# Optimization experiments

Measured on AMD Instinct MI355X. Metric: run time of the kernel, lower is better.

Reference implementation:

```python
import jax, jax.numpy as jnp
import numpy as np

EPS = 1e-5
H = 8  # num_heads


def _layernorm(x, g, b):
    m = x.mean(axis=-1, keepdims=True)
    v = jnp.mean((x - m) ** 2, axis=-1, keepdims=True)
    return (x - m) / jnp.sqrt(v + EPS) * g + b


def setup_inputs() -> dict:
    key = jax.random.key(0)
    ks = jax.random.split(key, 8)
    B, T, N, D, L = 4, 4096, 512, 1024, 768
    x = jax.random.normal(ks[0], (B, T, D), dtype=jnp.float32)
    cond = jax.random.normal(ks[1], (B, N, L), dtype=jnp.float32)
    # LayerNorm params
    ln_g = jnp.ones((D,), jnp.float32)
    ln_b = jnp.zeros((D,), jnp.float32)
    tln_g = jnp.ones((L,), jnp.float32)
    tln_b = jnp.zeros((L,), jnp.float32)
    # Linear params, stored as (in, out)
    Wq = jax.random.normal(ks[2], (D, D), jnp.float32) * 0.02
    bq = jnp.zeros((D,), jnp.float32)
    Wk = jax.random.normal(ks[3], (L, D), jnp.float32) * 0.02
    bk = jnp.zeros((D,), jnp.float32)
    Wv = jax.random.normal(ks[4], (L, D), jnp.float32) * 0.02
    bv = jnp.zeros((D,), jnp.float32)
    return {"input_tensor": x, "condition_tensor": cond,
            "ln_g": ln_g, "ln_b": ln_b, "tln_g": tln_g, "tln_b": tln_b,
            "Wq": Wq, "bq": bq, "Wk": Wk, "bk": bk, "Wv": Wv, "bv": bv}


def reference(input_tensor, condition_tensor, ln_g, ln_b, tln_g, tln_b,
              Wq, bq, Wk, bk, Wv, bv):
    B, T, D = input_tensor.shape
    N = condition_tensor.shape[1]
    xn = _layernorm(input_tensor, ln_g, ln_b)            # [B,T,D]
    cn = _layernorm(condition_tensor, tln_g, tln_b)      # [B,N,L]
    q = jnp.einsum('btd,de->bte', xn, Wq) + bq           # [B,T,D]
    k = jnp.einsum('bnl,ld->bnd', cn, Wk) + bk           # [B,N,D]
    v = jnp.einsum('bnl,ld->bnd', cn, Wv) + bv           # [B,N,D]
    q = jax.nn.softmax(q.reshape(B, T, H, D // H), axis=-1)  # softmax over head_dim
    k = jax.nn.softmax(k.reshape(B, N, H, D // H), axis=1)   # softmax over N
    v = v.reshape(B, N, H, D // H)
    context = jnp.einsum('bnhk,bnhv->bhkv', k, v)        # [B,H,hd,hd]
    y = jnp.einsum('bthk,bhkv->bthv', q, context).reshape(B, T, D)
    return y
```

## Files before the change

### kernel.cpp

```cpp
#include <hip/hip_runtime.h>
#include <hip/hip_bf16.h>
#include <stdint.h>

#define BATCH 4
#define TLEN  4096
#define DDIM  1024
#define NCOND 512
#define LDIM  768
#define NHEAD 8
#define HD    128

typedef __bf16 bf16x8 __attribute__((ext_vector_type(8)));
typedef float  f32x4  __attribute__((ext_vector_type(4)));

__device__ __forceinline__ unsigned short f2b(float f) {
    unsigned int u = __builtin_bit_cast(unsigned int, f);
    unsigned int r = (u + 0x7fffu + ((u >> 16) & 1u)) >> 16;
    return (unsigned short)r;
}
__device__ __forceinline__ float b2f(unsigned short s) {
    unsigned int u = ((unsigned int)s) << 16;
    return __builtin_bit_cast(float, u);
}

__device__ __forceinline__ void gl2lds(const void* g, void* l) {
    __builtin_amdgcn_global_load_lds(
        (const __attribute__((address_space(1))) void*)(uintptr_t)g,
        (__attribute__((address_space(3))) void*)(uintptr_t)l,
        16, 0, 0);
}

template<int NCH>
__device__ __forceinline__ void ln_row(const float* __restrict__ x,
    const float* __restrict__ g, const float* __restrict__ bb,
    unsigned short* __restrict__ o, long r, int lane)
{
    const int rowlen = NCH * 256;
    const float* p = x + r * (long)rowlen;
    float4 v[NCH];
    float s = 0.f, ss = 0.f;
#pragma unroll
    for (int i = 0; i < NCH; i++) {
        v[i] = *(const float4*)(p + i * 256 + lane * 4);
        s  += v[i].x + v[i].y + v[i].z + v[i].w;
        ss += v[i].x * v[i].x + v[i].y * v[i].y + v[i].z * v[i].z + v[i].w * v[i].w;
    }
#pragma unroll
    for (int off = 32; off; off >>= 1) {
        s  += __shfl_xor(s,  off, 64);
        ss += __shfl_xor(ss, off, 64);
    }
    float mu = s / rowlen;
    float rs = rsqrtf(fmaxf(ss / rowlen - mu * mu, 0.f) + 1e-5f);
    unsigned short* po = o + r * (long)rowlen;
#pragma unroll
    for (int i = 0; i < NCH; i++) {
        int c = i * 256 + lane * 4;
        float4 gv = *(const float4*)(g + c);
        float4 bv = *(const float4*)(bb + c);
        ushort4 o4;
        o4.x = f2b((v[i].x - mu) * rs * gv.x + bv.x);
        o4.y = f2b((v[i].y - mu) * rs * gv.y + bv.y);
        o4.z = f2b((v[i].z - mu) * rs * gv.z + bv.z);
        o4.w = f2b((v[i].w - mu) * rs * gv.w + bv.w);
        *(ushort4*)(po + c) = o4;
    }
}

__global__ __launch_bounds__(256) void prep(
    const float* __restrict__ x, const float* __restrict__ ln_g,
    const float* __restrict__ ln_b,
    const float* __restrict__ cond, const float* __restrict__ tln_g,
    const float* __restrict__ tln_b,
    const float* __restrict__ Wq, const float* __restrict__ Wk,
    const float* __restrict__ Wv,
    unsigned short* __restrict__ xn, unsigned short* __restrict__ cn,
    unsigned short* __restrict__ wqT, unsigned short* __restrict__ wkvT)
{
    int blk = blockIdx.x;
    int tid = threadIdx.x, wid = tid >> 6, lane = tid & 63;
    if (blk < 4096) {
        ln_row<4>(x, ln_g, ln_b, xn, (long)blk * 4 + wid, lane);
        return;
    }
    if (blk < 4608) {
        ln_row<3>(cond, tln_g, tln_b, cn, (long)(blk - 4096) * 4 + wid, lane);
        return;
    }
    int w = blk - 4608;
    const float* W; unsigned short* Wt; int K, wi;
    if (w < 1024)      { W = Wq; Wt = wqT;               K = DDIM; wi = w; }
    else if (w < 1792) { W = Wk; Wt = wkvT;              K = LDIM; wi = w - 1024; }
    else               { W = Wv; Wt = wkvT + 768 * 1024; K = LDIM; wi = w - 1792; }
    int n0 = (wi & 31) * 32, k0 = (wi >> 5) * 32;
    __shared__ float t[32][33];
    int tx = tid & 31, ty = tid >> 5;
#pragma unroll
    for (int i = 0; i < 4; i++)
        t[ty + i * 8][tx] = W[(long)(k0 + ty + i * 8) * DDIM + n0 + tx];
    __syncthreads();
#pragma unroll
    for (int i = 0; i < 4; i++)
        Wt[(long)(n0 + ty + i * 8) * K + k0 + tx] = f2b(t[tx][ty + i * 8]);
}

__global__ __launch_bounds__(256) void gemm_kv(
    const unsigned short* __restrict__ A,
    const unsigned short* __restrict__ Bt,
    const float* __restrict__ bk, const float* __restrict__ bv,
    float* __restrict__ Ck,
    unsigned short* __restrict__ Cvv)
{
    int zi = blockIdx.z;
    const unsigned short* Bp = Bt + (long)zi * 1024 * LDIM;
    const float* bias = zi ? bv : bk;

    int m0 = blockIdx.y * 128, n0 = blockIdx.x * 128;
    int tid = threadIdx.x, lane = tid & 63, wid = tid >> 6;
    int l16 = lane & 15, quad = lane >> 4;
    int mw = (wid & 1) << 6, nw = (wid >> 1) << 6;

    __shared__ unsigned short sb[16384];

    f32x4 acc[4][4];
#pragma unroll
    for (int i = 0; i < 4; i++)
#pragma unroll
        for (int j = 0; j < 4; j++) { acc[i][j][0] = 0.f; acc[i][j][1] = 0.f; acc[i][j][2] = 0.f; acc[i][j][3] = 0.f; }

    int cg = (tid & 3) ^ ((tid >> 3) & 3);
    const unsigned short* ag = A  + (long)(m0 + (tid >> 2)) * LDIM + cg * 8;
    const unsigned short* bg = Bp + (long)(n0 + (tid >> 2)) * LDIM + cg * 8;
    const long a64 = 64L * LDIM;
    int wsl = wid * 512;
    int sw = (l16 >> 1) & 3;

    auto stage = [&](unsigned short* d, int ko) {
        gl2lds(ag + ko,        d + wsl);
        gl2lds(ag + a64 + ko,  d + wsl + 2048);
        gl2lds(bg + ko,        d + 4096 + wsl);
        gl2lds(bg + a64 + ko,  d + 4096 + wsl + 2048);
    };

    const int NT = LDIM >> 5;
    stage(sb, 0);
    stage(sb + 8192, 32);

    for (int t = 0; t < NT; ++t) {
        if (t + 1 < NT) asm volatile("s_waitcnt vmcnt(4)" ::: "memory");
        else            asm volatile("s_waitcnt vmcnt(0)" ::: "memory");
        __builtin_amdgcn_s_barrier();
        __builtin_amdgcn_sched_barrier(0);
        unsigned short* Ac = sb + (t & 1) * 8192;
        bf16x8 af[4], bfr[4];
#pragma unroll
        for (int i = 0; i < 4; i++)
            af[i] = *(const bf16x8*)&Ac[(mw + i * 16 + l16) * 32 + ((quad ^ sw) * 8)];
#pragma unroll
        for (int j = 0; j < 4; j++)
            bfr[j] = *(const bf16x8*)&Ac[4096 + (nw + j * 16 + l16) * 32 + ((quad ^ sw) * 8)];
#pragma unroll
        for (int i = 0; i < 4; i++)
#pragma unroll
            for (int j = 0; j < 4; j++)
                acc[i][j] = __builtin_amdgcn_mfma_f32_16x16x32_bf16(af[i], bfr[j], acc[i][j], 0, 0, 0);
        __builtin_amdgcn_s_barrier();
        __builtin_amdgcn_sched_barrier(0);
        if (t + 2 < NT) stage(Ac, (t + 2) << 5);
    }

#pragma unroll
    for (int j = 0; j < 4; j++) {
        int col = n0 + nw + j * 16 + l16;
        float bvv = bias[col];
#pragma unroll
        for (int i = 0; i < 4; i++) {
            int row0 = m0 + mw + i * 16 + (quad << 2);
#pragma unroll
            for (int r = 0; r < 4; r++) {
                float val = acc[i][j][r] + bvv;
                long idx = (long)(row0 + r) * DDIM + col;
                if (zi == 0) Ck[idx]  = val;
                else         Cvv[idx] = f2b(val);
            }
        }
    }
}

__global__ __launch_bounds__(256) void ctx_mfma2s(const float* __restrict__ kraw,
    const unsigned short* __restrict__ v,
    unsigned short* __restrict__ ctxT)
{
    __shared__ unsigned short vT[128 * 72];
    __shared__ unsigned short kT[32 * 72];
    __shared__ float shm[8][33], shs[8][33];
    __shared__ float Mc[32], Sc[32];
    int kk0 = blockIdx.x * 32;
    int bh  = blockIdx.y;
    int b = bh >> 3, h = bh & 7;
    int tid = threadIdx.x, lane = tid & 63, wid = tid >> 6;
    int l16 = lane & 15, quad = lane >> 4;

    const float* kbase = kraw + (long)b * NCOND * DDIM + h * HD + kk0;

    {
        int c = tid & 31, seg = tid >> 5;
        float m = -1e30f, s = 0.f;
#pragma unroll 4
        for (int i = 0; i < 64; i++) {
            float val = kbase[(long)(seg * 64 + i) * DDIM + c];
            float nm = fmaxf(m, val);
            s = s * __expf(m - nm) + __expf(val - nm);
            m = nm;
        }
        shm[seg][c] = m; shs[seg][c] = s;
        __syncthreads();
        if (seg == 0) {
            float M = shm[0][c], S = shs[0][c];
#pragma unroll
            for (int t = 1; t < 8; t++) {
                float m2 = shm[t][c], s2 = shs[t][c];
                float nm = fmaxf(M, m2);
                S = S * __expf(M - nm) + s2 * __expf(m2 - nm);
                M = nm;
            }
            Mc[c] = M; Sc[c] = 1.f / S;
        }
        __syncthreads();
    }

    f32x4 acc[2][2];
#pragma unroll
    for (int i = 0; i < 2; i++)
#pragma unroll
        for (int j = 0; j < 2; j++) { acc[i][j][0] = 0.f; acc[i][j][1] = 0.f; acc[i][j][2] = 0.f; acc[i][j][3] = 0.f; }

    for (int s = 0; s < 8; s++) {
        int n0 = s * 64;
        const float* kp = kbase + (long)n0 * DDIM;
        const unsigned short* vp = v + (long)b * NCOND * DDIM + (long)n0 * DDIM + h * HD;
#pragma unroll
        for (int p = 0; p < 8; p++) {
            int e = p * 256 + tid;
            int nn = e >> 5, kk = e & 31;
            float val = __expf(kp[(long)nn * DDIM + kk] - Mc[kk]) * Sc[kk];
            kT[kk * 72 + nn] = f2b(val);
        }
#pragma unroll
        for (int p = 0; p < 16; p++) {
            int e = p * 256 + tid;
            int nn = e >> 6, v2 = (e & 63) * 2;
            unsigned int w = *(const unsigned int*)&vp[(long)nn * DDIM + v2];
            vT[v2 * 72 + nn]       = (unsigned short)w;
            vT[(v2 + 1) * 72 + nn] = (unsigned short)(w >> 16);
        }
        __syncthreads();
#pragma unroll
        for (int ks = 0; ks < 2; ks++) {
            bf16x8 af[2], bfr[2];
#pragma unroll
            for (int i = 0; i < 2; i++)
                af[i] = *(const bf16x8*)&vT[(wid * 32 + i * 16 + l16) * 72 + ks * 32 + quad * 8];
#pragma unroll
            for (int j = 0; j < 2; j++)
                bfr[j] = *(const bf16x8*)&kT[(j * 16 + l16) * 72 + ks * 32 + quad * 8];
#pragma unroll
            for (int i = 0; i < 2; i++)
#pragma unroll
                for (int j = 0; j < 2; j++)
                    acc[i][j] = __builtin_amdgcn_mfma_f32_16x16x32_bf16(af[i], bfr[j], acc[i][j], 0, 0, 0);
        }
        __syncthreads();
    }

    unsigned short* cp = ctxT + ((long)bh << 14);
#pragma unroll
    for (int i = 0; i < 2; i++)
#pragma unroll
        for (int j = 0; j < 2; j++)
#pragma unroll
            for (int r = 0; r < 4; r++)
                cp[(wid * 32 + i * 16 + quad * 4 + r) * 128 + kk0 + j * 16 + l16] =
                    f2b(acc[i][j][r]);
}

__global__ __launch_bounds__(256, 4) void qfused(
    const unsigned short* __restrict__ xn,
    const unsigned short* __restrict__ wqT,
    const float* __restrict__ bq,
    const unsigned short* __restrict__ ctxT,
    float* __restrict__ out)
{
    __shared__ unsigned short buf[18432];
    unsigned short* Pb = buf;
    float* redM = (float*)(buf + 17408);
    float* redS = redM + 256;

    int d = blockIdx.x;
    int xcd = d & 7, slot = d >> 3;
    int mtile = xcd * 16 + (slot >> 3);
    int head = slot & 7;
    int m0 = mtile * 128;
    int b  = m0 >> 12;
    int tid = threadIdx.x, lane = tid & 63, wid = tid >> 6;
    int l16 = lane & 15, quad = lane >> 4;
    int mw = (wid & 1) << 6, nw = (wid >> 1) << 6;
    int ch = wid >> 1;

    const unsigned short* cg2 = ctxT + ((long)(b * NHEAD + head) << 14);

    f32x4 acc[4][4];
#pragma unroll
    for (int i = 0; i < 4; i++)
#pragma unroll
        for (int j = 0; j < 4; j++) { acc[i][j][0] = 0.f; acc[i][j][1] = 0.f; acc[i][j][2] = 0.f; acc[i][j][3] = 0.f; }

    int cgs = (tid & 3) ^ ((tid >> 3) & 3);
    const unsigned short* ag = xn  + (long)(m0 + (tid >> 2)) * DDIM + cgs * 8;
    const unsigned short* bg = wqT + (long)(head * 128 + (tid >> 2)) * DDIM + cgs * 8;
    const long a64 = 64L * DDIM;
    int wsl = wid * 512;
    int sw = (l16 >> 1) & 3;

    auto stage = [&](unsigned short* dst, int ko) {
        gl2lds(ag + ko,        dst + wsl);
        gl2lds(ag + a64 + ko,  dst + wsl + 2048);
        gl2lds(bg + ko,        dst + 4096 + wsl);
        gl2lds(bg + a64 + ko,  dst + 4096 + wsl + 2048);
    };

    const int NT = DDIM >> 5;
    stage(buf, 0);
    stage(buf + 8192, 32);

    for (int t = 0; t < NT; ++t) {
        if (t + 1 < NT) asm volatile("s_waitcnt vmcnt(4)" ::: "memory");
        else            asm volatile("s_waitcnt vmcnt(0)" ::: "memory");
        __builtin_amdgcn_s_barrier();
        __builtin_amdgcn_sched_barrier(0);
        unsigned short* Ac = buf + (t & 1) * 8192;
        bf16x8 af[4], bfr[4];
#pragma unroll
        for (int i = 0; i < 4; i++)
            af[i] = *(const bf16x8*)&Ac[(mw + i * 16 + l16) * 32 + ((quad ^ sw) * 8)];
#pragma unroll
        for (int j = 0; j < 4; j++)
            bfr[j] = *(const bf16x8*)&Ac[4096 + (nw + j * 16 + l16) * 32 + ((quad ^ sw) * 8)];
        __builtin_amdgcn_s_setprio(1);
#pragma unroll
        for (int i = 0; i < 4; i++)
#pragma unroll
            for (int j = 0; j < 4; j++)
                acc[i][j] = __builtin_amdgcn_mfma_f32_16x16x32_bf16(af[i], bfr[j], acc[i][j], 0, 0, 0);
        __builtin_amdgcn_s_setprio(0);
        __builtin_amdgcn_s_barrier();
        __builtin_amdgcn_sched_barrier(0);
        if (t + 2 < NT) stage(Ac, (t + 2) << 5);
    }

    float bvv[4];
#pragma unroll
    for (int j = 0; j < 4; j++) bvv[j] = bq[head * 128 + nw + j * 16 + l16];
#pragma unroll
    for (int i = 0; i < 4; i++)
#pragma unroll
        for (int j = 0; j < 4; j++)
#pragma unroll
            for (int r = 0; r < 4; r++) acc[i][j][r] += bvv[j];

    float mx[4][4];
#pragma unroll
    for (int i = 0; i < 4; i++)
#pragma unroll
        for (int r = 0; r < 4; r++) {
            float m = acc[i][0][r];
            m = fmaxf(m, acc[i][1][r]);
            m = fmaxf(m, acc[i][2][r]);
            m = fmaxf(m, acc[i][3][r]);
            mx[i][r] = m;
        }
#pragma unroll
    for (int off = 1; off < 16; off <<= 1)
#pragma unroll
        for (int i = 0; i < 4; i++)
#pragma unroll
            for (int r = 0; r < 4; r++)
                mx[i][r] = fmaxf(mx[i][r], __shfl_xor(mx[i][r], off, 64));
    if (l16 == 0) {
#pragma unroll
        for (int i = 0; i < 4; i++)
#pragma unroll
            for (int r = 0; r < 4; r++)
                redM[ch * 128 + mw + i * 16 + quad * 4 + r] = mx[i][r];
    }
    __syncthreads();

    float sm[4][4];
#pragma unroll
    for (int i = 0; i < 4; i++)
#pragma unroll
        for (int r = 0; r < 4; r++) {
            int row = mw + i * 16 + quad * 4 + r;
            float M = fmaxf(redM[row], redM[128 + row]);
            float s = 0.f;
#pragma unroll
            for (int j = 0; j < 4; j++) {
                unsigned short eb = f2b(__expf(acc[i][j][r] - M));
                Pb[row * 136 + nw + j * 16 + l16] = eb;
                s += b2f(eb);
            }
            sm[i][r] = s;
        }
#pragma unroll
    for (int off = 1; off < 16; off <<= 1)
#pragma unroll
        for (int i = 0; i < 4; i++)
#pragma unroll
            for (int r = 0; r < 4; r++)
                sm[i][r] += __shfl_xor(sm[i][r], off, 64);
    if (l16 == 0) {
#pragma unroll
        for (int i = 0; i < 4; i++)
#pragma unroll
            for (int r = 0; r < 4; r++)
                redS[ch * 128 + mw + i * 16 + quad * 4 + r] = sm[i][r];
    }
    __syncthreads();

    f32x4 acc2[4][4];
#pragma unroll
    for (int i = 0; i < 4; i++)
#pragma unroll
        for (int j = 0; j < 4; j++) { acc2[i][j][0] = 0.f; acc2[i][j][1] = 0.f; acc2[i][j][2] = 0.f; acc2[i][j][3] = 0.f; }
#pragma unroll
    for (int ks = 0; ks < 4; ks++) {
        bf16x8 af[4], bfr[4];
#pragma unroll
        for (int j = 0; j < 4; j++)
            bfr[j] = *(const bf16x8*)&cg2[(nw + j * 16 + l16) * 128 + ks * 32 + quad * 8];
#pragma unroll
        for (int i = 0; i < 4; i++)
            af[i] = *(const bf16x8*)&Pb[(mw + i * 16 + l16) * 136 + ks * 32 + quad * 8];
#pragma unroll
        for (int i = 0; i < 4; i++)
#pragma unroll
            for (int j = 0; j < 4; j++)
                acc2[i][j] = __builtin_amdgcn_mfma_f32_16x16x32_bf16(af[i], bfr[j], acc2[i][j], 0, 0, 0);
    }

#pragma unroll
    for (int i = 0; i < 4; i++)
#pragma unroll
        for (int r = 0; r < 4; r++) {
            int row = mw + i * 16 + quad * 4 + r;
            float invd = 1.f / (redS[row] + redS[128 + row]);
            float* op = out + (long)(m0 + row) * DDIM + head * 128;
#pragma unroll
            for (int j = 0; j < 4; j++)
                op[nw + j * 16 + l16] = acc2[i][j][r] * invd;
        }
}

extern "C" void kernel_launch(void* const* d_in, const int* in_sizes, int n_in,
                              void* d_out, int out_size, void* d_ws, size_t ws_size,
                              hipStream_t stream) {
    (void)in_sizes; (void)n_in; (void)out_size; (void)ws_size;
    const float* x     = (const float*)d_in[0];
    const float* cond  = (const float*)d_in[1];
    const float* ln_g  = (const float*)d_in[2];
    const float* ln_b  = (const float*)d_in[3];
    const float* tln_g = (const float*)d_in[4];
    const float* tln_b = (const float*)d_in[5];
    const float* Wq    = (const float*)d_in[6];
    const float* bq    = (const float*)d_in[7];
    const float* Wk    = (const float*)d_in[8];
    const float* bk    = (const float*)d_in[9];
    const float* Wv    = (const float*)d_in[10];
    const float* bv    = (const float*)d_in[11];
    float* out = (float*)d_out;

    uint8_t* w8 = (uint8_t*)d_ws;
    unsigned short* xn   = (unsigned short*)w8;
    unsigned short* cn   = (unsigned short*)(w8 + 33554432);
    unsigned short* wqT  = (unsigned short*)(w8 + 36700160);
    unsigned short* wkvT = (unsigned short*)(w8 + 38797312);
    float*          fk   = (float*)(w8 + 41943040);
    unsigned short* fvb  = (unsigned short*)(w8 + 50331648);
    unsigned short* ctxT = (unsigned short*)(w8 + 56623104);

    prep<<<7168, 256, 0, stream>>>(x, ln_g, ln_b, cond, tln_g, tln_b,
                                   Wq, Wk, Wv, xn, cn, wqT, wkvT);
    gemm_kv<<<dim3(8, 16, 2), 256, 0, stream>>>(cn, wkvT, bk, bv, fk, fvb);
    ctx_mfma2s<<<dim3(4, 32), 256, 0, stream>>>(fk, fvb, ctxT);
    qfused<<<1024, 256, 0, stream>>>(xn, wqT, bq, ctxT, out);
}
```

Before: 242.1 us.

## Vectorize weight transpose, reorder gemm_kv grid, double ctx kernel block count

The weight-transpose part of prep now uses 64x64 tiles with float4 loads and ushort4 stores instead of 32x32 scalar tiles, which cuts the block count and widens memory transactions. gemm_kv swaps the grid axes so that consecutive blocks walk along M instead of N, changing cache reuse order. ctx_mfma2s now gives each block 16 key columns instead of 32, doubling the grid from 128 to 256 blocks to fill more CUs. The price is that each ctx block reloads the full V slice, so total V traffic doubles.

After: 263.3 us. 8.8% more time.

```diff
diff --git a/kernel.cpp b/kernel.cpp
--- a/kernel.cpp
+++ b/kernel.cpp
@@ -89,19 +89,28 @@
     }
     int w = blk - 4608;
     const float* W; unsigned short* Wt; int K, wi;
-    if (w < 1024)      { W = Wq; Wt = wqT;               K = DDIM; wi = w; }
-    else if (w < 1792) { W = Wk; Wt = wkvT;              K = LDIM; wi = w - 1024; }
-    else               { W = Wv; Wt = wkvT + 768 * 1024; K = LDIM; wi = w - 1792; }
-    int n0 = (wi & 31) * 32, k0 = (wi >> 5) * 32;
-    __shared__ float t[32][33];
-    int tx = tid & 31, ty = tid >> 5;
-#pragma unroll
-    for (int i = 0; i < 4; i++)
-        t[ty + i * 8][tx] = W[(long)(k0 + ty + i * 8) * DDIM + n0 + tx];
+    if (w < 256)      { W = Wq; Wt = wqT;               K = DDIM; wi = w; }
+    else if (w < 448) { W = Wk; Wt = wkvT;              K = LDIM; wi = w - 256; }
+    else              { W = Wv; Wt = wkvT + 768 * 1024; K = LDIM; wi = w - 448; }
+    int n0 = (wi & 15) * 64, k0 = (wi >> 4) * 64;
+    __shared__ float t[64][65];
+    int tx4 = (tid & 15) * 4, ty = tid >> 4;
+#pragma unroll
+    for (int i = 0; i < 4; i++) {
+        int kr = ty + i * 16;
+        float4 v4 = *(const float4*)&W[(long)(k0 + kr) * DDIM + n0 + tx4];
+        t[kr][tx4 + 0] = v4.x; t[kr][tx4 + 1] = v4.y;
+        t[kr][tx4 + 2] = v4.z; t[kr][tx4 + 3] = v4.w;
+    }
     __syncthreads();
 #pragma unroll
-    for (int i = 0; i < 4; i++)
-        Wt[(long)(n0 + ty + i * 8) * K + k0 + tx] = f2b(t[tx][ty + i * 8]);
+    for (int i = 0; i < 4; i++) {
+        int nr = ty + i * 16;
+        ushort4 o4;
+        o4.x = f2b(t[tx4 + 0][nr]); o4.y = f2b(t[tx4 + 1][nr]);
+        o4.z = f2b(t[tx4 + 2][nr]); o4.w = f2b(t[tx4 + 3][nr]);
+        *(ushort4*)&Wt[(long)(n0 + nr) * K + k0 + tx4] = o4;
+    }
 }
 
 __global__ __launch_bounds__(256) void gemm_kv(
@@ -115,7 +124,7 @@
     const unsigned short* Bp = Bt + (long)zi * 1024 * LDIM;
     const float* bias = zi ? bv : bk;
 
-    int m0 = blockIdx.y * 128, n0 = blockIdx.x * 128;
+    int m0 = blockIdx.x * 128, n0 = blockIdx.y * 128;
     int tid = threadIdx.x, lane = tid & 63, wid = tid >> 6;
     int l16 = lane & 15, quad = lane >> 4;
     int mw = (wid & 1) << 6, nw = (wid >> 1) << 6;
@@ -192,10 +201,10 @@
     unsigned short* __restrict__ ctxT)
 {
     __shared__ unsigned short vT[128 * 72];
-    __shared__ unsigned short kT[32 * 72];
-    __shared__ float shm[8][33], shs[8][33];
-    __shared__ float Mc[32], Sc[32];
-    int kk0 = blockIdx.x * 32;
+    __shared__ unsigned short kT[16 * 72];
+    __shared__ float shm[16][17], shs[16][17];
+    __shared__ float Mc[16], Sc[16];
+    int kk0 = blockIdx.x * 16;
     int bh  = blockIdx.y;
     int b = bh >> 3, h = bh & 7;
     int tid = threadIdx.x, lane = tid & 63, wid = tid >> 6;
@@ -204,11 +213,11 @@
     const float* kbase = kraw + (long)b * NCOND * DDIM + h * HD + kk0;
 
     {
-        int c = tid & 31, seg = tid >> 5;
+        int c = tid & 15, seg = tid >> 4;
         float m = -1e30f, s = 0.f;
 #pragma unroll 4
-        for (int i = 0; i < 64; i++) {
-            float val = kbase[(long)(seg * 64 + i) * DDIM + c];
+        for (int i = 0; i < 32; i++) {
+            float val = kbase[(long)(seg * 32 + i) * DDIM + c];
             float nm = fmaxf(m, val);
             s = s * __expf(m - nm) + __expf(val - nm);
             m = nm;
@@ -218,7 +227,7 @@
         if (seg == 0) {
             float M = shm[0][c], S = shs[0][c];
 #pragma unroll
-            for (int t = 1; t < 8; t++) {
+            for (int t = 1; t < 16; t++) {
                 float m2 = shm[t][c], s2 = shs[t][c];
                 float nm = fmaxf(M, m2);
                 S = S * __expf(M - nm) + s2 * __expf(m2 - nm);
@@ -229,20 +238,18 @@
         __syncthreads();
     }
 
-    f32x4 acc[2][2];
-#pragma unroll
-    for (int i = 0; i < 2; i++)
-#pragma unroll
-        for (int j = 0; j < 2; j++) { acc[i][j][0] = 0.f; acc[i][j][1] = 0.f; acc[i][j][2] = 0.f; acc[i][j][3] = 0.f; }
+    f32x4 acc[2];
+#pragma unroll
+    for (int i = 0; i < 2; i++) { acc[i][0] = 0.f; acc[i][1] = 0.f; acc[i][2] = 0.f; acc[i][3] = 0.f; }
 
     for (int s = 0; s < 8; s++) {
         int n0 = s * 64;
         const float* kp = kbase + (long)n0 * DDIM;
         const unsigned short* vp = v + (long)b * NCOND * DDIM + (long)n0 * DDIM + h * HD;
 #pragma unroll
-        for (int p = 0; p < 8; p++) {
+        for (int p = 0; p < 4; p++) {
             int e = p * 256 + tid;
-            int nn = e >> 5, kk = e & 31;
+            int nn = e >> 4, kk = e & 15;
             float val = __expf(kp[(long)nn * DDIM + kk] - Mc[kk]) * Sc[kk];
             kT[kk * 72 + nn] = f2b(val);
         }
@@ -257,18 +264,14 @@
         __syncthreads();
 #pragma unroll
         for (int ks = 0; ks < 2; ks++) {
-            bf16x8 af[2], bfr[2];
+            bf16x8 af[2], bfr;
 #pragma unroll
             for (int i = 0; i < 2; i++)
                 af[i] = *(const bf16x8*)&vT[(wid * 32 + i * 16 + l16) * 72 + ks * 32 + quad * 8];
-#pragma unroll
-            for (int j = 0; j < 2; j++)
-                bfr[j] = *(const bf16x8*)&kT[(j * 16 + l16) * 72 + ks * 32 + quad * 8];
+            bfr = *(const bf16x8*)&kT[l16 * 72 + ks * 32 + quad * 8];
 #pragma unroll
             for (int i = 0; i < 2; i++)
-#pragma unroll
-                for (int j = 0; j < 2; j++)
-                    acc[i][j] = __builtin_amdgcn_mfma_f32_16x16x32_bf16(af[i], bfr[j], acc[i][j], 0, 0, 0);
+                acc[i] = __builtin_amdgcn_mfma_f32_16x16x32_bf16(af[i], bfr, acc[i], 0, 0, 0);
         }
         __syncthreads();
     }
@@ -277,11 +280,8 @@
 #pragma unroll
     for (int i = 0; i < 2; i++)
 #pragma unroll
-        for (int j = 0; j < 2; j++)
-#pragma unroll
-            for (int r = 0; r < 4; r++)
-                cp[(wid * 32 + i * 16 + quad * 4 + r) * 128 + kk0 + j * 16 + l16] =
-                    f2b(acc[i][j][r]);
+        for (int r = 0; r < 4; r++)
+            cp[(wid * 32 + i * 16 + quad * 4 + r) * 128 + kk0 + l16] = f2b(acc[i][r]);
 }
 
 __global__ __launch_bounds__(256, 4) void qfused(
@@ -488,9 +488,9 @@
     unsigned short* fvb  = (unsigned short*)(w8 + 50331648);
     unsigned short* ctxT = (unsigned short*)(w8 + 56623104);
 
-    prep<<<7168, 256, 0, stream>>>(x, ln_g, ln_b, cond, tln_g, tln_b,
+    prep<<<5248, 256, 0, stream>>>(x, ln_g, ln_b, cond, tln_g, tln_b,
                                    Wq, Wk, Wv, xn, cn, wqT, wkvT);
-    gemm_kv<<<dim3(8, 16, 2), 256, 0, stream>>>(cn, wkvT, bk, bv, fk, fvb);
-    ctx_mfma2s<<<dim3(4, 32), 256, 0, stream>>>(fk, fvb, ctxT);
+    gemm_kv<<<dim3(16, 8, 2), 256, 0, stream>>>(cn, wkvT, bk, bv, fk, fvb);
+    ctx_mfma2s<<<dim3(8, 32), 256, 0, stream>>>(fk, fvb, ctxT);
     qfused<<<1024, 256, 0, stream>>>(xn, wqT, bq, ctxT, out);
 }
```

## Enlarge Q-projection fused tile to 256x256 with 8 waves and interleaved prefetch

Applied to the files above, without the earlier changes.

The fused Q GEMM + softmax + context kernel now uses 512-thread blocks, each covering a 256-row by 256-column (two-head) tile with a 64-wide K step, in place of 128x128 tiles over 256 threads. The next K tile's global-to-LDS loads are issued in quarters between the MFMA phases. The aim is more data reuse per LDS load and less redundant traffic for xn and Wq. The cost is a much larger LDS footprint (~140 KB), a full vmcnt(0) wait each iteration, many extra barriers, and only 256 blocks, which lowers occupancy and parallelism.

Result: faster. 229.4 us (-5.2%).

```diff
diff --git a/kernel.cpp b/kernel.cpp
--- a/kernel.cpp
+++ b/kernel.cpp
@@ -284,129 +284,151 @@
                     f2b(acc[i][j][r]);
 }
 
-__global__ __launch_bounds__(256, 4) void qfused(
+__global__ __launch_bounds__(512, 2) void qfused2(
     const unsigned short* __restrict__ xn,
     const unsigned short* __restrict__ wqT,
     const float* __restrict__ bq,
     const unsigned short* __restrict__ ctxT,
     float* __restrict__ out)
 {
-    __shared__ unsigned short buf[18432];
-    unsigned short* Pb = buf;
-    float* redM = (float*)(buf + 17408);
-    float* redS = redM + 256;
+    __shared__ unsigned short buf[71680];
+    unsigned short* sbA = buf;
+    unsigned short* sbB = buf + 32768;
+    unsigned short* Pb  = buf;
+    float* redM = (float*)(buf + 67584);
+    float* redS = redM + 1024;
 
     int d = blockIdx.x;
-    int xcd = d & 7, slot = d >> 3;
-    int mtile = xcd * 16 + (slot >> 3);
-    int head = slot & 7;
-    int m0 = mtile * 128;
+    int swz = (d & 7) * 32 + (d >> 3);
+    int mt = swz >> 2, hp = swz & 3;
+    int m0 = mt * 256;
     int b  = m0 >> 12;
+
     int tid = threadIdx.x, lane = tid & 63, wid = tid >> 6;
     int l16 = lane & 15, quad = lane >> 4;
-    int mw = (wid & 1) << 6, nw = (wid >> 1) << 6;
-    int ch = wid >> 1;
-
-    const unsigned short* cg2 = ctxT + ((long)(b * NHEAD + head) << 14);
-
-    f32x4 acc[4][4];
-#pragma unroll
-    for (int i = 0; i < 4; i++)
+    int wm = wid & 1, wn = wid >> 1;
+    int h  = wn >> 1;
+
+    f32x4 acc[8][4];
+#pragma unroll
+    for (int i = 0; i < 8; i++)
 #pragma unroll
         for (int j = 0; j < 4; j++) { acc[i][j][0] = 0.f; acc[i][j][1] = 0.f; acc[i][j][2] = 0.f; acc[i][j][3] = 0.f; }
 
-    int cgs = (tid & 3) ^ ((tid >> 3) & 3);
-    const unsigned short* ag = xn  + (long)(m0 + (tid >> 2)) * DDIM + cgs * 8;
-    const unsigned short* bg = wqT + (long)(head * 128 + (tid >> 2)) * DDIM + cgs * 8;
-    const long a64 = 64L * DDIM;
-    int wsl = wid * 512;
-    int sw = (l16 >> 1) & 3;
-
-    auto stage = [&](unsigned short* dst, int ko) {
-        gl2lds(ag + ko,        dst + wsl);
-        gl2lds(ag + a64 + ko,  dst + wsl + 2048);
-        gl2lds(bg + ko,        dst + 4096 + wsl);
-        gl2lds(bg + a64 + ko,  dst + 4096 + wsl + 2048);
+    int cgs  = (tid & 7) ^ ((tid >> 3) & 7);
+    int rsub = tid >> 3;
+    int ldsb = rsub * 64 + (tid & 7) * 8;
+    const unsigned short* agb = xn  + (long)(m0 + rsub) * DDIM + cgs * 8;
+    const unsigned short* bgb = wqT + (long)(hp * 256 + rsub) * DDIM + cgs * 8;
+
+    auto stageA = [&](int t1, int hh) {
+        unsigned short* dst = sbA + (t1 & 1) * 16384 + hh * 8192 + ldsb;
+        const unsigned short* g = agb + (long)(hh * 128) * DDIM + t1 * 64;
+        gl2lds(g, dst);
+        gl2lds(g + 64L * DDIM, dst + 4096);
     };
-
-    const int NT = DDIM >> 5;
-    stage(buf, 0);
-    stage(buf + 8192, 32);
-
+    auto stageB = [&](int t1, int hh) {
+        unsigned short* dst = sbB + (t1 & 1) * 16384 + hh * 8192 + ldsb;
+        const unsigned short* g = bgb + (long)(hh * 128) * DDIM + t1 * 64;
+        gl2lds(g, dst);
+        gl2lds(g + 64L * DDIM, dst + 4096);
+    };
+
+    stageA(0, 0); stageA(0, 1); stageB(0, 0); stageB(0, 1);
+
+    int sl7 = l16 & 7;
+    const int NT = DDIM >> 6;
     for (int t = 0; t < NT; ++t) {
-        if (t + 1 < NT) asm volatile("s_waitcnt vmcnt(4)" ::: "memory");
-        else            asm volatile("s_waitcnt vmcnt(0)" ::: "memory");
+        asm volatile("s_waitcnt vmcnt(0)" ::: "memory");
         __builtin_amdgcn_s_barrier();
         __builtin_amdgcn_sched_barrier(0);
-        unsigned short* Ac = buf + (t & 1) * 8192;
-        bf16x8 af[4], bfr[4];
-#pragma unroll
-        for (int i = 0; i < 4; i++)
-            af[i] = *(const bf16x8*)&Ac[(mw + i * 16 + l16) * 32 + ((quad ^ sw) * 8)];
+        const unsigned short* A = sbA + (t & 1) * 16384;
+        const unsigned short* B = sbB + (t & 1) * 16384;
+        bool pf = (t + 1 < NT);
+#pragma unroll
+        for (int ks = 0; ks < 2; ++ks) {
+            int slot = ((ks * 4 + quad) ^ sl7) * 8;
+            bf16x8 bfr[4];
+#pragma unroll
+            for (int j = 0; j < 4; ++j)
+                bfr[j] = *(const bf16x8*)&B[(wn * 64 + j * 16 + l16) * 64 + slot];
+#pragma unroll
+            for (int mh = 0; mh < 2; ++mh) {
+                bf16x8 af[4];
+#pragma unroll
+                for (int ii = 0; ii < 4; ++ii)
+                    af[ii] = *(const bf16x8*)&A[(wm * 128 + (mh * 4 + ii) * 16 + l16) * 64 + slot];
+                if (pf) {
+                    int ph = ks * 2 + mh;
+                    if      (ph == 0) stageA(t + 1, 0);
+                    else if (ph == 1) stageA(t + 1, 1);
+                    else if (ph == 2) stageB(t + 1, 0);
+                    else              stageB(t + 1, 1);
+                }
+                __builtin_amdgcn_s_barrier();
+                asm volatile("s_waitcnt lgkmcnt(0)" ::: "memory");
+                __builtin_amdgcn_sched_barrier(0);
+                __builtin_amdgcn_s_setprio(1);
+#pragma unroll
+                for (int ii = 0; ii < 4; ++ii)
+#pragma unroll
+                    for (int j = 0; j < 4; ++j)
+                        acc[mh * 4 + ii][j] = __builtin_amdgcn_mfma_f32_16x16x32_bf16(
+                            af[ii], bfr[j], acc[mh * 4 + ii][j], 0, 0, 0);
+                __builtin_amdgcn_s_setprio(0);
+                __builtin_amdgcn_s_barrier();
+                __builtin_amdgcn_sched_barrier(0);
+            }
+        }
+    }
+
+    float bvv[4];
+#pragma unroll
+    for (int j = 0; j < 4; j++) bvv[j] = bq[hp * 256 + wn * 64 + j * 16 + l16];
+#pragma unroll
+    for (int i = 0; i < 8; i++)
 #pragma unroll
         for (int j = 0; j < 4; j++)
-            bfr[j] = *(const bf16x8*)&Ac[4096 + (nw + j * 16 + l16) * 32 + ((quad ^ sw) * 8)];
-        __builtin_amdgcn_s_setprio(1);
-#pragma unroll
-        for (int i = 0; i < 4; i++)
-#pragma unroll
-            for (int j = 0; j < 4; j++)
-                acc[i][j] = __builtin_amdgcn_mfma_f32_16x16x32_bf16(af[i], bfr[j], acc[i][j], 0, 0, 0);
-        __builtin_amdgcn_s_setprio(0);
-        __builtin_amdgcn_s_barrier();
-        __builtin_amdgcn_sched_barrier(0);
-        if (t + 2 < NT) stage(Ac, (t + 2) << 5);
-    }
-
-    float bvv[4];
-#pragma unroll
-    for (int j = 0; j < 4; j++) bvv[j] = bq[head * 128 + nw + j * 16 + l16];
-#pragma unroll
-    for (int i = 0; i < 4; i++)
-#pragma unroll
-        for (int j = 0; j < 4; j++)
 #pragma unroll
             for (int r = 0; r < 4; r++) acc[i][j][r] += bvv[j];
 
-    float mx[4][4];
-#pragma unroll
-    for (int i = 0; i < 4; i++)
+    float mx[8][4];
+#pragma unroll
+    for (int i = 0; i < 8; i++)
 #pragma unroll
         for (int r = 0; r < 4; r++) {
-            float m = acc[i][0][r];
-            m = fmaxf(m, acc[i][1][r]);
-            m = fmaxf(m, acc[i][2][r]);
-            m = fmaxf(m, acc[i][3][r]);
+            float m = fmaxf(fmaxf(acc[i][0][r], acc[i][1][r]),
+                            fmaxf(acc[i][2][r], acc[i][3][r]));
             mx[i][r] = m;
         }
 #pragma unroll
     for (int off = 1; off < 16; off <<= 1)
 #pragma unroll
-        for (int i = 0; i < 4; i++)
+        for (int i = 0; i < 8; i++)
 #pragma unroll
             for (int r = 0; r < 4; r++)
                 mx[i][r] = fmaxf(mx[i][r], __shfl_xor(mx[i][r], off, 64));
     if (l16 == 0) {
 #pragma unroll
-        for (int i = 0; i < 4; i++)
+        for (int i = 0; i < 8; i++)
 #pragma unroll
             for (int r = 0; r < 4; r++)
-                redM[ch * 128 + mw + i * 16 + quad * 4 + r] = mx[i][r];
+                redM[wn * 256 + wm * 128 + i * 16 + quad * 4 + r] = mx[i][r];
     }
     __syncthreads();
 
-    float sm[4][4];
-#pragma unroll
-    for (int i = 0; i < 4; i++)
+    float sm[8][4];
+#pragma unroll
+    for (int i = 0; i < 8; i++)
 #pragma unroll
         for (int r = 0; r < 4; r++) {
-            int row = mw + i * 16 + quad * 4 + r;
-            float M = fmaxf(redM[row], redM[128 + row]);
+            int row = wm * 128 + i * 16 + quad * 4 + r;
+            float M = fmaxf(redM[(h * 2) * 256 + row], redM[(h * 2 + 1) * 256 + row]);
             float s = 0.f;
 #pragma unroll
             for (int j = 0; j < 4; j++) {
                 unsigned short eb = f2b(__expf(acc[i][j][r] - M));
-                Pb[row * 136 + nw + j * 16 + l16] = eb;
+                Pb[row * 264 + wn * 64 + j * 16 + l16] = eb;
                 s += b2f(eb);
             }
             sm[i][r] = s;
@@ -414,50 +436,50 @@
 #pragma unroll
     for (int off = 1; off < 16; off <<= 1)
 #pragma unroll
-        for (int i = 0; i < 4; i++)
+        for (int i = 0; i < 8; i++)
 #pragma unroll
             for (int r = 0; r < 4; r++)
                 sm[i][r] += __shfl_xor(sm[i][r], off, 64);
     if (l16 == 0) {
 #pragma unroll
-        for (int i = 0; i < 4; i++)
+        for (int i = 0; i < 8; i++)
 #pragma unroll
             for (int r = 0; r < 4; r++)
-                redS[ch * 128 + mw + i * 16 + quad * 4 + r] = sm[i][r];
+                redS[wn * 256 + wm * 128 + i * 16 + quad * 4 + r] = sm[i][r];
     }
     __syncthreads();
 
-    f32x4 acc2[4][4];
-#pragma unroll
-    for (int i = 0; i < 4; i++)
+    const unsigned short* cg2 = ctxT + ((long)(b * NHEAD + hp * 2 + h) << 14);
+    f32x4 acc2[8][4];
+#pragma unroll
+    for (int i = 0; i < 8; i++)
 #pragma unroll
         for (int j = 0; j < 4; j++) { acc2[i][j][0] = 0.f; acc2[i][j][1] = 0.f; acc2[i][j][2] = 0.f; acc2[i][j][3] = 0.f; }
 #pragma unroll
     for (int ks = 0; ks < 4; ks++) {
-        bf16x8 af[4], bfr[4];
+        bf16x8 bfr2[4];
 #pragma unroll
         for (int j = 0; j < 4; j++)
-            bfr[j] = *(const bf16x8*)&cg2[(nw + j * 16 + l16) * 128 + ks * 32 + quad * 8];
-#pragma unroll
-        for (int i = 0; i < 4; i++)
-            af[i] = *(const bf16x8*)&Pb[(mw + i * 16 + l16) * 136 + ks * 32 + quad * 8];
-#pragma unroll
-        for (int i = 0; i < 4; i++)
+            bfr2[j] = *(const bf16x8*)&cg2[((wn & 1) * 64 + j * 16 + l16) * 128 + ks * 32 + quad * 8];
+#pragma unroll
+        for (int i = 0; i < 8; i++) {
+            bf16x8 af2 = *(const bf16x8*)&Pb[(wm * 128 + i * 16 + l16) * 264 + h * 128 + ks * 32 + quad * 8];
 #pragma unroll
             for (int j = 0; j < 4; j++)
-                acc2[i][j] = __builtin_amdgcn_mfma_f32_16x16x32_bf16(af[i], bfr[j], acc2[i][j], 0, 0, 0);
-    }
-
-#pragma unroll
-    for (int i = 0; i < 4; i++)
+                acc2[i][j] = __builtin_amdgcn_mfma_f32_16x16x32_bf16(af2, bfr2[j], acc2[i][j], 0, 0, 0);
+        }
+    }
+
+#pragma unroll
+    for (int i = 0; i < 8; i++)
 #pragma unroll
         for (int r = 0; r < 4; r++) {
-            int row = mw + i * 16 + quad * 4 + r;
-            float invd = 1.f / (redS[row] + redS[128 + row]);
-            float* op = out + (long)(m0 + row) * DDIM + head * 128;
+            int row = wm * 128 + i * 16 + quad * 4 + r;
+            float invd = 1.f / (redS[(h * 2) * 256 + row] + redS[(h * 2 + 1) * 256 + row]);
+            float* op = out + (long)(m0 + row) * DDIM + hp * 256;
 #pragma unroll
             for (int j = 0; j < 4; j++)
-                op[nw + j * 16 + l16] = acc2[i][j][r] * invd;
+                op[wn * 64 + j * 16 + l16] = acc2[i][j][r] * invd;
         }
 }
 
@@ -492,5 +514,5 @@
                                    Wq, Wk, Wv, xn, cn, wqT, wkvT);
     gemm_kv<<<dim3(8, 16, 2), 256, 0, stream>>>(cn, wkvT, bk, bv, fk, fvb);
     ctx_mfma2s<<<dim3(4, 32), 256, 0, stream>>>(fk, fvb, ctxT);
-    qfused<<<1024, 256, 0, stream>>>(xn, wqT, bq, ctxT, out);
-}
+    qfused2<<<256, 512, 0, stream>>>(xn, wqT, bq, ctxT, out);
+}
```
